# Kernel tuning notes

Hardware: AMD Instinct MI355X
Metric: run time of the kernel (lower is better)

The kernel has to match this reference:

```python
import jax, jax.numpy as jnp
import numpy as np

B, S, D = 2048, 200, 128   # batch, n_steps, embedding dim per vector
H = 64                      # hidden_dim
MASK_SCALE = 1e10


def setup_inputs() -> dict:
    key = jax.random.key(0)
    ks = jax.random.split(key, 6)
    his = jax.random.normal(ks[0], (B, S, D), dtype=jnp.float32)
    target = jax.random.normal(ks[1], (B, 1, D), dtype=jnp.float32)
    # mask == 1.0 marks padded history positions (they get -1e10 added pre-softmax)
    mask = (jax.random.uniform(ks[2], (B, S)) < 0.3).astype(jnp.float32)
    W = jax.random.normal(ks[3], (3 * D, H), dtype=jnp.float32) * 0.1
    W_bias = jnp.full((H,), 0.1, dtype=jnp.float32)
    O = jax.random.normal(ks[4], (H, 1), dtype=jnp.float32) * 0.1
    O_bias = jnp.full((1,), 0.1, dtype=jnp.float32)
    return {"his": his, "target": target, "mask": mask,
            "W": W, "W_bias": W_bias, "O": O, "O_bias": O_bias}


def reference(his, target, mask, W, W_bias, O, O_bias):
    tgt = jnp.broadcast_to(target, his.shape)          # [B,S,D] tile over steps
    diff = his - tgt
    att_vec = jnp.concatenate([his, diff, tgt], axis=2)  # [B,S,3D]
    h = jax.nn.relu(jnp.einsum('bsf,fh->bsh', att_vec, W) + W_bias)  # [B,S,H]
    alpha = jnp.einsum('bsh,ho->bso', h, O) + O_bias   # [B,S,1]
    alpha = alpha[:, :, 0] - mask * MASK_SCALE         # [B,S]
    attn = jax.nn.softmax(alpha, axis=-1)              # [B,S]
    out = jnp.einsum('bs,bsd->bd', attn, his)          # weighted-sum pooling
    return out
```

## Files before the change

### kernel.cpp

```cpp
#include <hip/hip_runtime.h>

#define B_ 2048
#define S_ 200
#define D_ 128
#define H_ 64
#define MASK_SCALE 1e10f

typedef __attribute__((ext_vector_type(8))) short short8_t;
typedef __attribute__((ext_vector_type(4))) float f32x4;
typedef __attribute__((ext_vector_type(4))) unsigned short ushort4_t;

__device__ __forceinline__ unsigned short f2bf(float f) {
    unsigned u = __float_as_uint(f);
    unsigned r = (u + 0x7fffu + ((u >> 16) & 1u)) >> 16;
    return (unsigned short)r;
}
__device__ __forceinline__ float bf2f(unsigned short v) {
    return __uint_as_float(((unsigned)v) << 16);
}
__device__ __forceinline__ unsigned cvt_pk_bf16(float lo, float hi) {
    unsigned r;
    asm("v_cvt_pk_bf16_f32 %0, %1, %2" : "=v"(r) : "v"(lo), "v"(hi));
    return r;
}

__global__ __launch_bounds__(256) void prep(const float* __restrict__ W,
                                            unsigned short* __restrict__ wfrag,
                                            float* __restrict__ w23t) {
    int idx = blockIdx.x * 256 + threadIdx.x;
    int d = idx >> 6;
    int h = idx & 63;
    float w1 = W[d * H_ + h];
    float w2 = W[(D_ + d) * H_ + h];
    float w3 = W[(2 * D_ + d) * H_ + h];
    int kt = d >> 5, q = (d >> 3) & 3, j = d & 7;
    int nt = h >> 4, lm = h & 15;
    int lane = (q << 4) | lm;
    wfrag[((kt * 4 + nt) * 64 + lane) * 8 + j] = f2bf(w1 + w2);
    w23t[h * D_ + d] = w3 - w2;
}

__global__ __launch_bounds__(256, 3) void fused_kernel(const float* __restrict__ his,
                                                       const float* __restrict__ mask,
                                                       const float* __restrict__ target,
                                                       const float* __restrict__ W_bias,
                                                       const unsigned short* __restrict__ wfrag,
                                                       const float* __restrict__ w23t,
                                                       const float* __restrict__ Ovec,
                                                       float* __restrict__ out) {
    __shared__ unsigned short hisb[S_ * D_];
    __shared__ float alpha_s[208];
    __shared__ float red8[8];
    __shared__ float ov_s[H_];
    __shared__ float pool_s[3 * D_];
    float* tpp = pool_s;

    const int b    = blockIdx.x;
    const int t    = threadIdx.x;
    const int lane = t & 63;
    const int wv   = t >> 6;
    const int lm   = lane & 15;
    const int q    = lane >> 4;

    float mk = (t < S_) ? mask[(size_t)b * S_ + t] : 0.f;
    if (t < H_) ov_s[t] = Ovec[t];

    {
        float acc = (wv == 0) ? W_bias[lane] : 0.f;
        const float4* tg4 = (const float4*)(target + (size_t)b * D_) + wv * 8;
        const float4* wt4 = (const float4*)(w23t + lane * D_) + wv * 8;
        #pragma unroll
        for (int i = 0; i < 8; ++i) {
            float4 tv = tg4[i];
            float4 wc = wt4[i];
            acc = fmaf(tv.x, wc.x, acc);
            acc = fmaf(tv.y, wc.y, acc);
            acc = fmaf(tv.z, wc.z, acc);
            acc = fmaf(tv.w, wc.w, acc);
        }
        tpp[wv * 64 + lane] = acc;
    }

    short8_t bfrag[16];
    #pragma unroll
    for (int f = 0; f < 16; ++f)
        bfrag[f] = *(const short8_t*)(wfrag + ((size_t)(f * 64 + lane)) * 8);

    const float4* hb4 = (const float4*)(his + (size_t)b * S_ * D_);
    #pragma unroll
    for (int g = 0; g < 5; ++g) {
        float4 x[5];
        #pragma unroll
        for (int j = 0; j < 5; ++j)
            x[j] = hb4[t + (g * 5 + j) * 256];
        #pragma unroll
        for (int j = 0; j < 5; ++j) {
            int i  = t + (g * 5 + j) * 256;
            int s  = i >> 5;
            int d8 = i & 31;
            int pc = (d8 >> 1) ^ (s & 15);
            uint2 v;
            v.x = cvt_pk_bf16(x[j].x, x[j].y);
            v.y = cvt_pk_bf16(x[j].z, x[j].w);
            *(uint2*)((char*)hisb + s * 256 + pc * 16 + (d8 & 1) * 8) = v;
        }
    }
    __syncthreads();

    float th[4];
    #pragma unroll
    for (int nt = 0; nt < 4; ++nt) {
        int h = nt * 16 + lm;
        th[nt] = tpp[h] + tpp[64 + h] + tpp[128 + h] + tpp[192 + h];
    }

    for (int tile = wv; tile < 13; tile += 4) {
        int row0 = tile * 16;
        int ar = row0 + lm; if (ar > S_ - 1) ar = S_ - 1;

        f32x4 acc[4];
        #pragma unroll
        for (int nt = 0; nt < 4; ++nt) acc[nt] = (f32x4){0.f, 0.f, 0.f, 0.f};

        #pragma unroll
        for (int kt = 0; kt < 4; ++kt) {
            int c = (kt * 4 + q) ^ (ar & 15);
            short8_t a = *(const short8_t*)((const char*)hisb + ar * 256 + c * 16);
            #pragma unroll
            for (int nt = 0; nt < 4; ++nt)
                acc[nt] = __builtin_amdgcn_mfma_f32_16x16x32_bf16(a, bfrag[kt * 4 + nt], acc[nt], 0, 0, 0);
        }

        float part[4];
        #pragma unroll
        for (int r = 0; r < 4; ++r) {
            float sum = 0.f;
            #pragma unroll
            for (int nt = 0; nt < 4; ++nt) {
                int h = nt * 16 + lm;
                float v = acc[nt][r] + th[nt];
                v = fmaxf(v, 0.f);
                sum = fmaf(v, ov_s[h], sum);
            }
            part[r] = sum;
        }
        #pragma unroll
        for (int off = 1; off < 16; off <<= 1) {
            #pragma unroll
            for (int r = 0; r < 4; ++r)
                part[r] += __shfl_xor(part[r], off);
        }
        if (lm == 0) {
            #pragma unroll
            for (int r = 0; r < 4; ++r)
                alpha_s[row0 + q * 4 + r] = part[r];
        }
    }
    __syncthreads();

    float a = (t < S_) ? alpha_s[t] - mk * MASK_SCALE : -INFINITY;
    float m = a;
    #pragma unroll
    for (int off = 1; off < 64; off <<= 1) m = fmaxf(m, __shfl_xor(m, off));
    if (lane == 0) red8[wv] = m;
    __syncthreads();
    m = fmaxf(fmaxf(red8[0], red8[1]), fmaxf(red8[2], red8[3]));
    float e = (t < S_) ? __expf(a - m) : 0.f;
    float ssum = e;
    #pragma unroll
    for (int off = 1; off < 64; off <<= 1) ssum += __shfl_xor(ssum, off);
    if (lane == 0) red8[4 + wv] = ssum;
    __syncthreads();
    float inv = 1.f / (red8[4] + red8[5] + red8[6] + red8[7]);
    __syncthreads();
    if (t < S_) alpha_s[t] = e * inv;
    __syncthreads();

    const int d8 = t & 31;
    const int sg = t >> 5;
    float acc0 = 0.f, acc1 = 0.f, acc2 = 0.f, acc3 = 0.f;
    #pragma unroll 5
    for (int s = sg; s < S_; s += 8) {
        float w = alpha_s[s];
        int pc = (d8 >> 1) ^ (s & 15);
        ushort4_t v = *(const ushort4_t*)((const char*)hisb + s * 256 + pc * 16 + (d8 & 1) * 8);
        acc0 = fmaf(w, bf2f(v[0]), acc0);
        acc1 = fmaf(w, bf2f(v[1]), acc1);
        acc2 = fmaf(w, bf2f(v[2]), acc2);
        acc3 = fmaf(w, bf2f(v[3]), acc3);
    }
    acc0 += __shfl_xor(acc0, 32);
    acc1 += __shfl_xor(acc1, 32);
    acc2 += __shfl_xor(acc2, 32);
    acc3 += __shfl_xor(acc3, 32);
    if (wv && lane < 32) {
        float4 p; p.x = acc0; p.y = acc1; p.z = acc2; p.w = acc3;
        *(float4*)(&pool_s[(wv - 1) * D_ + d8 * 4]) = p;
    }
    __syncthreads();
    if (wv == 0 && lane < 32) {
        #pragma unroll
        for (int k = 0; k < 3; ++k) {
            const float4 p = *(const float4*)(&pool_s[k * D_ + d8 * 4]);
            acc0 += p.x; acc1 += p.y; acc2 += p.z; acc3 += p.w;
        }
        float4 o; o.x = acc0; o.y = acc1; o.z = acc2; o.w = acc3;
        *(float4*)(out + (size_t)b * D_ + d8 * 4) = o;
    }
}

extern "C" void kernel_launch(void* const* d_in, const int* in_sizes, int n_in,
                              void* d_out, int out_size, void* d_ws, size_t ws_size,
                              hipStream_t stream) {
    const float* his    = (const float*)d_in[0];
    const float* target = (const float*)d_in[1];
    const float* mask   = (const float*)d_in[2];
    const float* W      = (const float*)d_in[3];
    const float* W_bias = (const float*)d_in[4];
    const float* Ovec   = (const float*)d_in[5];
    float* out = (float*)d_out;

    char* ws = (char*)d_ws;
    unsigned short* wfrag = (unsigned short*)ws;
    float* w23t           = (float*)(ws + 16384);

    prep<<<32, 256, 0, stream>>>(W, wfrag, w23t);
    fused_kernel<<<B_, 256, 0, stream>>>(his, mask, target, W_bias, wfrag, w23t, Ovec, out);
}
```

Before: 313.8 us.

## Make fused kernel persistent over 8 batches with double-buffered LDS prefetch

Each 512-thread block now handles 8 consecutive batch rows. It double-buffers the bf16 history tile in LDS and issues the global loads for the next row before running the MFMA/softmax/pool work on the current one, so memory latency overlaps compute. Softmax normalisation moves to the final output scale, and weight fragments are loaded once per block instead of once per row. In exchange, register pressure rises from holding 13 prefetched float4 values, LDS use doubles to about 100KB per block, and only 256 blocks are launched, which may underfill the GPU.

```diff
diff --git a/kernel.cpp b/kernel.cpp
--- a/kernel.cpp
+++ b/kernel.cpp
@@ -4,6 +4,8 @@
 #define S_ 200
 #define D_ 128
 #define H_ 64
+#define KB_ 8
+#define GRID_ (B_ / KB_)
 #define MASK_SCALE 1e10f
 
 typedef __attribute__((ext_vector_type(8))) short short8_t;
@@ -22,6 +24,9 @@
     unsigned r;
     asm("v_cvt_pk_bf16_f32 %0, %1, %2" : "=v"(r) : "v"(lo), "v"(hi));
     return r;
+}
+__device__ __forceinline__ void bar() {
+    asm volatile("s_waitcnt lgkmcnt(0)\n\ts_barrier" ::: "memory");
 }
 
 __global__ __launch_bounds__(256) void prep(const float* __restrict__ W,
@@ -40,7 +45,7 @@
     w23t[h * D_ + d] = w3 - w2;
 }
 
-__global__ __launch_bounds__(256, 3) void fused_kernel(const float* __restrict__ his,
+__global__ __launch_bounds__(512, 2) void fused_kernel(const float* __restrict__ his,
                                                        const float* __restrict__ mask,
                                                        const float* __restrict__ target,
                                                        const float* __restrict__ W_bias,
@@ -48,164 +53,228 @@
                                                        const float* __restrict__ w23t,
                                                        const float* __restrict__ Ovec,
                                                        float* __restrict__ out) {
-    __shared__ unsigned short hisb[S_ * D_];
-    __shared__ float alpha_s[208];
+    __shared__ unsigned short hisb[2][S_ * D_];
+    __shared__ float alph[208];
+    __shared__ float attw[208];
     __shared__ float red8[8];
+    __shared__ float red8b[8];
     __shared__ float ov_s[H_];
-    __shared__ float pool_s[3 * D_];
-    float* tpp = pool_s;
-
-    const int b    = blockIdx.x;
+    __shared__ float tpp[8 * H_];
+    __shared__ float pool_s[7 * D_];
+
     const int t    = threadIdx.x;
     const int lane = t & 63;
     const int wv   = t >> 6;
     const int lm   = lane & 15;
     const int q    = lane >> 4;
-
-    float mk = (t < S_) ? mask[(size_t)b * S_ + t] : 0.f;
+    const int b0   = blockIdx.x * KB_;
+
     if (t < H_) ov_s[t] = Ovec[t];
-
-    {
-        float acc = (wv == 0) ? W_bias[lane] : 0.f;
-        const float4* tg4 = (const float4*)(target + (size_t)b * D_) + wv * 8;
-        const float4* wt4 = (const float4*)(w23t + lane * D_) + wv * 8;
-        #pragma unroll
-        for (int i = 0; i < 8; ++i) {
-            float4 tv = tg4[i];
-            float4 wc = wt4[i];
-            acc = fmaf(tv.x, wc.x, acc);
-            acc = fmaf(tv.y, wc.y, acc);
-            acc = fmaf(tv.z, wc.z, acc);
-            acc = fmaf(tv.w, wc.w, acc);
-        }
-        tpp[wv * 64 + lane] = acc;
-    }
+    const float wb = (wv == 0) ? W_bias[lane] : 0.f;
 
     short8_t bfrag[16];
     #pragma unroll
     for (int f = 0; f < 16; ++f)
         bfrag[f] = *(const short8_t*)(wfrag + ((size_t)(f * 64 + lane)) * 8);
-
-    const float4* hb4 = (const float4*)(his + (size_t)b * S_ * D_);
+    float4 wsl[4];
     #pragma unroll
-    for (int g = 0; g < 5; ++g) {
-        float4 x[5];
-        #pragma unroll
-        for (int j = 0; j < 5; ++j)
-            x[j] = hb4[t + (g * 5 + j) * 256];
-        #pragma unroll
-        for (int j = 0; j < 5; ++j) {
-            int i  = t + (g * 5 + j) * 256;
-            int s  = i >> 5;
-            int d8 = i & 31;
-            int pc = (d8 >> 1) ^ (s & 15);
-            uint2 v;
-            v.x = cvt_pk_bf16(x[j].x, x[j].y);
-            v.y = cvt_pk_bf16(x[j].z, x[j].w);
-            *(uint2*)((char*)hisb + s * 256 + pc * 16 + (d8 & 1) * 8) = v;
+    for (int k = 0; k < 4; ++k)
+        wsl[k] = *(const float4*)(w23t + lane * D_ + wv * 16 + k * 4);
+
+    float mk;
+    {
+        const float4* hb4 = (const float4*)(his + (size_t)b0 * S_ * D_);
+        float4 x0[13];
+        #pragma unroll
+        for (int j = 0; j < 13; ++j) {
+            int i = t + j * 512;
+            if (i < 6400) x0[j] = hb4[i];
+        }
+        mk = (t < S_) ? mask[(size_t)b0 * S_ + t] : 0.f;
+        const float4* tg4 = (const float4*)(target + (size_t)b0 * D_) + wv * 4;
+        float acc = wb;
+        #pragma unroll
+        for (int k = 0; k < 4; ++k) {
+            float4 tv = tg4[k];
+            acc = fmaf(tv.x, wsl[k].x, acc);
+            acc = fmaf(tv.y, wsl[k].y, acc);
+            acc = fmaf(tv.z, wsl[k].z, acc);
+            acc = fmaf(tv.w, wsl[k].w, acc);
+        }
+        tpp[wv * 64 + lane] = acc;
+        #pragma unroll
+        for (int j = 0; j < 13; ++j) {
+            int i = t + j * 512;
+            if (i < 6400) {
+                int s = i >> 5, d8 = i & 31;
+                int pc = (d8 >> 1) ^ (s & 15);
+                uint2 v;
+                v.x = cvt_pk_bf16(x0[j].x, x0[j].y);
+                v.y = cvt_pk_bf16(x0[j].z, x0[j].w);
+                *(uint2*)((char*)hisb[0] + s * 256 + pc * 16 + (d8 & 1) * 8) = v;
+            }
         }
     }
     __syncthreads();
 
-    float th[4];
-    #pragma unroll
-    for (int nt = 0; nt < 4; ++nt) {
-        int h = nt * 16 + lm;
-        th[nt] = tpp[h] + tpp[64 + h] + tpp[128 + h] + tpp[192 + h];
-    }
-
-    for (int tile = wv; tile < 13; tile += 4) {
-        int row0 = tile * 16;
-        int ar = row0 + lm; if (ar > S_ - 1) ar = S_ - 1;
-
-        f32x4 acc[4];
-        #pragma unroll
-        for (int nt = 0; nt < 4; ++nt) acc[nt] = (f32x4){0.f, 0.f, 0.f, 0.f};
-
-        #pragma unroll
-        for (int kt = 0; kt < 4; ++kt) {
-            int c = (kt * 4 + q) ^ (ar & 15);
-            short8_t a = *(const short8_t*)((const char*)hisb + ar * 256 + c * 16);
-            #pragma unroll
-            for (int nt = 0; nt < 4; ++nt)
-                acc[nt] = __builtin_amdgcn_mfma_f32_16x16x32_bf16(a, bfrag[kt * 4 + nt], acc[nt], 0, 0, 0);
-        }
-
-        float part[4];
-        #pragma unroll
-        for (int r = 0; r < 4; ++r) {
-            float sum = 0.f;
-            #pragma unroll
-            for (int nt = 0; nt < 4; ++nt) {
-                int h = nt * 16 + lm;
-                float v = acc[nt][r] + th[nt];
-                v = fmaxf(v, 0.f);
-                sum = fmaf(v, ov_s[h], sum);
-            }
-            part[r] = sum;
-        }
-        #pragma unroll
-        for (int off = 1; off < 16; off <<= 1) {
-            #pragma unroll
-            for (int r = 0; r < 4; ++r)
-                part[r] += __shfl_xor(part[r], off);
-        }
-        if (lm == 0) {
-            #pragma unroll
-            for (int r = 0; r < 4; ++r)
-                alpha_s[row0 + q * 4 + r] = part[r];
-        }
-    }
-    __syncthreads();
-
-    float a = (t < S_) ? alpha_s[t] - mk * MASK_SCALE : -INFINITY;
-    float m = a;
-    #pragma unroll
-    for (int off = 1; off < 64; off <<= 1) m = fmaxf(m, __shfl_xor(m, off));
-    if (lane == 0) red8[wv] = m;
-    __syncthreads();
-    m = fmaxf(fmaxf(red8[0], red8[1]), fmaxf(red8[2], red8[3]));
-    float e = (t < S_) ? __expf(a - m) : 0.f;
-    float ssum = e;
-    #pragma unroll
-    for (int off = 1; off < 64; off <<= 1) ssum += __shfl_xor(ssum, off);
-    if (lane == 0) red8[4 + wv] = ssum;
-    __syncthreads();
-    float inv = 1.f / (red8[4] + red8[5] + red8[6] + red8[7]);
-    __syncthreads();
-    if (t < S_) alpha_s[t] = e * inv;
-    __syncthreads();
-
-    const int d8 = t & 31;
-    const int sg = t >> 5;
-    float acc0 = 0.f, acc1 = 0.f, acc2 = 0.f, acc3 = 0.f;
-    #pragma unroll 5
-    for (int s = sg; s < S_; s += 8) {
-        float w = alpha_s[s];
-        int pc = (d8 >> 1) ^ (s & 15);
-        ushort4_t v = *(const ushort4_t*)((const char*)hisb + s * 256 + pc * 16 + (d8 & 1) * 8);
-        acc0 = fmaf(w, bf2f(v[0]), acc0);
-        acc1 = fmaf(w, bf2f(v[1]), acc1);
-        acc2 = fmaf(w, bf2f(v[2]), acc2);
-        acc3 = fmaf(w, bf2f(v[3]), acc3);
-    }
-    acc0 += __shfl_xor(acc0, 32);
-    acc1 += __shfl_xor(acc1, 32);
-    acc2 += __shfl_xor(acc2, 32);
-    acc3 += __shfl_xor(acc3, 32);
-    if (wv && lane < 32) {
-        float4 p; p.x = acc0; p.y = acc1; p.z = acc2; p.w = acc3;
-        *(float4*)(&pool_s[(wv - 1) * D_ + d8 * 4]) = p;
-    }
-    __syncthreads();
-    if (wv == 0 && lane < 32) {
-        #pragma unroll
-        for (int k = 0; k < 3; ++k) {
-            const float4 p = *(const float4*)(&pool_s[k * D_ + d8 * 4]);
-            acc0 += p.x; acc1 += p.y; acc2 += p.z; acc3 += p.w;
-        }
-        float4 o; o.x = acc0; o.y = acc1; o.z = acc2; o.w = acc3;
-        *(float4*)(out + (size_t)b * D_ + d8 * 4) = o;
+    int cur = 0;
+    for (int n = 0; n < KB_; ++n) {
+        const int b = b0 + n;
+        const bool more = (n + 1 < KB_);
+        const unsigned short* hb = hisb[cur];
+
+        float th[4];
+        #pragma unroll
+        for (int nt = 0; nt < 4; ++nt) {
+            int h = nt * 16 + lm;
+            float s0 = tpp[h] + tpp[64 + h] + tpp[128 + h] + tpp[192 + h];
+            float s1 = tpp[256 + h] + tpp[320 + h] + tpp[384 + h] + tpp[448 + h];
+            th[nt] = s0 + s1;
+        }
+
+        float4 x[13];
+        float4 tg[4];
+        float mkn = 0.f;
+        if (more) {
+            const float4* hb4n = (const float4*)(his + (size_t)(b + 1) * S_ * D_);
+            #pragma unroll
+            for (int j = 0; j < 13; ++j) {
+                int i = t + j * 512;
+                if (i < 6400) x[j] = hb4n[i];
+            }
+            const float4* tg4 = (const float4*)(target + (size_t)(b + 1) * D_) + wv * 4;
+            #pragma unroll
+            for (int k = 0; k < 4; ++k) tg[k] = tg4[k];
+            if (t < S_) mkn = mask[(size_t)(b + 1) * S_ + t];
+        }
+
+        #pragma unroll
+        for (int tt = 0; tt < 2; ++tt) {
+            int tile = wv + tt * 8;
+            if (tile < 13) {
+                int row0 = tile * 16;
+                int ar = row0 + lm; if (ar > S_ - 1) ar = S_ - 1;
+
+                f32x4 acc[4];
+                #pragma unroll
+                for (int nt = 0; nt < 4; ++nt) acc[nt] = (f32x4){0.f, 0.f, 0.f, 0.f};
+                #pragma unroll
+                for (int kt = 0; kt < 4; ++kt) {
+                    int c = (kt * 4 + q) ^ (ar & 15);
+                    short8_t av = *(const short8_t*)((const char*)hb + ar * 256 + c * 16);
+                    #pragma unroll
+                    for (int nt = 0; nt < 4; ++nt)
+                        acc[nt] = __builtin_amdgcn_mfma_f32_16x16x32_bf16(av, bfrag[kt * 4 + nt], acc[nt], 0, 0, 0);
+                }
+                float part[4];
+                #pragma unroll
+                for (int r = 0; r < 4; ++r) {
+                    float sum = 0.f;
+                    #pragma unroll
+                    for (int nt = 0; nt < 4; ++nt) {
+                        int h = nt * 16 + lm;
+                        float v = acc[nt][r] + th[nt];
+                        v = fmaxf(v, 0.f);
+                        sum = fmaf(v, ov_s[h], sum);
+                    }
+                    part[r] = sum;
+                }
+                #pragma unroll
+                for (int off = 1; off < 16; off <<= 1) {
+                    #pragma unroll
+                    for (int r = 0; r < 4; ++r)
+                        part[r] += __shfl_xor(part[r], off);
+                }
+                if (lm == 0) {
+                    #pragma unroll
+                    for (int r = 0; r < 4; ++r)
+                        alph[row0 + q * 4 + r] = part[r];
+                }
+            }
+        }
+        bar();
+
+        float a = (t < S_) ? alph[t] - mk * MASK_SCALE : -INFINITY;
+        float m = a;
+        #pragma unroll
+        for (int off = 1; off < 64; off <<= 1) m = fmaxf(m, __shfl_xor(m, off));
+        if (lane == 0) red8[wv] = m;
+        bar();
+        m = red8[0];
+        #pragma unroll
+        for (int k = 1; k < 8; ++k) m = fmaxf(m, red8[k]);
+        float e = (t < S_) ? __expf(a - m) : 0.f;
+        if (t < S_) attw[t] = e;
+        float ssum = e;
+        #pragma unroll
+        for (int off = 1; off < 64; off <<= 1) ssum += __shfl_xor(ssum, off);
+        if (lane == 0) red8b[wv] = ssum;
+        bar();
+        float tot = red8b[0];
+        #pragma unroll
+        for (int k = 1; k < 8; ++k) tot += red8b[k];
+        const float inv = 1.f / tot;
+
+        const int d8 = t & 31;
+        const int sg = t >> 5;
+        float acc0 = 0.f, acc1 = 0.f, acc2 = 0.f, acc3 = 0.f;
+        for (int s = sg; s < S_; s += 16) {
+            float w = attw[s];
+            int pc = (d8 >> 1) ^ (s & 15);
+            ushort4_t v = *(const ushort4_t*)((const char*)hb + s * 256 + pc * 16 + (d8 & 1) * 8);
+            acc0 = fmaf(w, bf2f(v[0]), acc0);
+            acc1 = fmaf(w, bf2f(v[1]), acc1);
+            acc2 = fmaf(w, bf2f(v[2]), acc2);
+            acc3 = fmaf(w, bf2f(v[3]), acc3);
+        }
+        acc0 += __shfl_xor(acc0, 32);
+        acc1 += __shfl_xor(acc1, 32);
+        acc2 += __shfl_xor(acc2, 32);
+        acc3 += __shfl_xor(acc3, 32);
+        if (wv && lane < 32) {
+            float4 p; p.x = acc0; p.y = acc1; p.z = acc2; p.w = acc3;
+            *(float4*)(&pool_s[(wv - 1) * D_ + d8 * 4]) = p;
+        }
+
+        if (more) {
+            unsigned short* hn = hisb[cur ^ 1];
+            #pragma unroll
+            for (int j = 0; j < 13; ++j) {
+                int i = t + j * 512;
+                if (i < 6400) {
+                    int s = i >> 5, d8c = i & 31;
+                    int pc = (d8c >> 1) ^ (s & 15);
+                    uint2 v;
+                    v.x = cvt_pk_bf16(x[j].x, x[j].y);
+                    v.y = cvt_pk_bf16(x[j].z, x[j].w);
+                    *(uint2*)((char*)hn + s * 256 + pc * 16 + (d8c & 1) * 8) = v;
+                }
+            }
+            float acc = wb;
+            #pragma unroll
+            for (int k = 0; k < 4; ++k) {
+                acc = fmaf(tg[k].x, wsl[k].x, acc);
+                acc = fmaf(tg[k].y, wsl[k].y, acc);
+                acc = fmaf(tg[k].z, wsl[k].z, acc);
+                acc = fmaf(tg[k].w, wsl[k].w, acc);
+            }
+            tpp[wv * 64 + lane] = acc;
+        }
+        bar();
+
+        if (wv == 0 && lane < 32) {
+            #pragma unroll
+            for (int k = 0; k < 7; ++k) {
+                const float4 p = *(const float4*)(&pool_s[k * D_ + d8 * 4]);
+                acc0 += p.x; acc1 += p.y; acc2 += p.z; acc3 += p.w;
+            }
+            float4 o;
+            o.x = acc0 * inv; o.y = acc1 * inv; o.z = acc2 * inv; o.w = acc3 * inv;
+            *(float4*)(out + (size_t)b * D_ + d8 * 4) = o;
+        }
+
+        mk = mkn;
+        cur ^= 1;
     }
 }
 
@@ -225,5 +294,5 @@
     float* w23t           = (float*)(ws + 16384);
 
     prep<<<32, 256, 0, stream>>>(W, wfrag, w23t);
-    fused_kernel<<<B_, 256, 0, stream>>>(his, mask, target, W_bias, wfrag, w23t, Ovec, out);
-}
+    fused_kernel<<<GRID_, 512, 0, stream>>>(his, mask, target, W_bias, wfrag, w23t, Ovec, out);
+}
```

Measured after the change: 302.5 us. 1.04x faster.
